# Optimization experiments

Hardware: AMD Instinct MI355X
Metric: run time of the kernel (lower is better)

Reference implementation:

```python
import math
import jax, jax.numpy as jnp
import numpy as np

D_MODEL = 512
NHEAD = 8
D_HEAD = D_MODEL // NHEAD
ATTN_TEMP = 1.0
B, LQ, LK = 2, 2048, 4096


def _linear_params(key, d_in, d_out):
    kw, kb = jax.random.split(key)
    bound = 1.0 / math.sqrt(d_in)
    W = jax.random.uniform(kw, (d_out, d_in), jnp.float32, -bound, bound)
    b = jax.random.uniform(kb, (d_out,), jnp.float32, -bound, bound)
    return W, b


def setup_inputs() -> dict:
    key = jax.random.key(0)
    ks = jax.random.split(key, 8)
    q = jax.random.normal(ks[0], (B, LQ, D_MODEL), jnp.float32)
    kv = jax.random.normal(ks[1], (B, LK, D_MODEL), jnp.float32)
    key_gate = jax.random.uniform(ks[2], (B, LK), jnp.float32)
    key_mask = jax.random.randint(ks[3], (B, LK), 0, 2, jnp.int32)
    Wq, bq = _linear_params(ks[4], D_MODEL, D_MODEL)
    Wk, bk = _linear_params(ks[5], D_MODEL, D_MODEL)
    Wv, bv = _linear_params(ks[6], D_MODEL, D_MODEL)
    Wo, bo = _linear_params(ks[7], D_MODEL, D_MODEL)
    return {"q": q, "kv": kv, "key_gate": key_gate, "key_mask": key_mask,
            "Wq": Wq, "bq": bq, "Wk": Wk, "bk": bk,
            "Wv": Wv, "bv": bv, "Wo": Wo, "bo": bo}


def reference(q, kv, key_gate, key_mask, Wq, bq, Wk, bk, Wv, bv, Wo, bo):
    Bq, Lq, _ = q.shape
    _, Lk, _ = kv.shape
    # projections -> (B, H, L, Dh)
    qp = (q @ Wq.T + bq).reshape(Bq, Lq, NHEAD, D_HEAD).transpose(0, 2, 1, 3)
    kp = (kv @ Wk.T + bk).reshape(Bq, Lk, NHEAD, D_HEAD).transpose(0, 2, 1, 3)
    vp = (kv @ Wv.T + bv).reshape(Bq, Lk, NHEAD, D_HEAD).transpose(0, 2, 1, 3)
    # scores: (B, H, Lq, Lk)
    scores = jnp.einsum('bhqd,bhkd->bhqk', qp, kp) / (math.sqrt(D_HEAD) * ATTN_TEMP)
    log_gate = jnp.log(jnp.clip(key_gate, 1e-6, None))  # (B, Lk)
    scores = scores + log_gate[:, None, None, :]
    pad = (key_mask == 0)[:, None, None, :]
    scores = jnp.where(pad, -jnp.inf, scores)
    attn = jax.nn.softmax(scores, axis=-1)  # dropout is identity in eval
    out = jnp.einsum('bhqk,bhkd->bhqd', attn, vp)
    out = out.transpose(0, 2, 1, 3).reshape(Bq, Lq, D_MODEL)
    return out @ Wo.T + bo
```

## Files before the change

### kernel.cpp

```cpp
#include <hip/hip_runtime.h>
#include <hip/hip_bf16.h>


using bf16   = __hip_bfloat16;
using bf16x8 = __attribute__((ext_vector_type(8))) short;
using f32x4  = __attribute__((ext_vector_type(4))) float;
using f32x16 = __attribute__((ext_vector_type(16))) float;
using uint4v = __attribute__((ext_vector_type(4))) unsigned int;

#define MFMA16(a, b, c) __builtin_amdgcn_mfma_f32_16x16x32_bf16((a), (b), (c), 0, 0, 0)
#define MFMA32(a, b, c) __builtin_amdgcn_mfma_f32_32x32x16_bf16((a), (b), (c), 0, 0, 0)

__device__ __forceinline__ bf16x8 load8(const bf16* p) {
    return *reinterpret_cast<const bf16x8*>(p);
}
__device__ __forceinline__ short f2bf(float x) {
    bf16 h = __float2bfloat16(x);
    return *reinterpret_cast<short*>(&h);
}

__global__ void cvt_x(const float* __restrict__ q, const float* __restrict__ kv,
                      bf16* __restrict__ qb, bf16* __restrict__ kvb) {
    int i = blockIdx.x * blockDim.x + threadIdx.x;
    const float* src; bf16* dst; int j;
    if (i < 524288) { src = q;  dst = qb;  j = i; }
    else            { src = kv; dst = kvb; j = i - 524288; }
    float4 v = reinterpret_cast<const float4*>(src)[j];
    ushort4 o;
    o.x = (unsigned short)f2bf(v.x);
    o.y = (unsigned short)f2bf(v.y);
    o.z = (unsigned short)f2bf(v.z);
    o.w = (unsigned short)f2bf(v.w);
    reinterpret_cast<ushort4*>(dst)[j] = o;
}

__global__ void cvt_w(const float* __restrict__ a, const float* __restrict__ b,
                      const float* __restrict__ c, const float* __restrict__ d,
                      bf16* __restrict__ oa, bf16* __restrict__ ob,
                      bf16* __restrict__ oc, bf16* __restrict__ od) {
    int i = blockIdx.x * blockDim.x + threadIdx.x;
    int t = i >> 16, j = i & 65535;
    const float* src = (t == 0) ? a : (t == 1) ? b : (t == 2) ? c : d;
    bf16*        dst = (t == 0) ? oa : (t == 1) ? ob : (t == 2) ? oc : od;
    float4 v = reinterpret_cast<const float4*>(src)[j];
    ushort4 o;
    o.x = (unsigned short)f2bf(v.x);
    o.y = (unsigned short)f2bf(v.y);
    o.z = (unsigned short)f2bf(v.z);
    o.w = (unsigned short)f2bf(v.w);
    reinterpret_cast<ushort4*>(dst)[j] = o;
}

__global__ void prep_gate_kernel(const float* __restrict__ gate,
                                 const int* __restrict__ mask,
                                 float* __restrict__ g, int n) {
    int i = blockIdx.x * blockDim.x + threadIdx.x;
    if (i < n) {
        float gv = fmaxf(gate[i], 1e-6f);
        g[i] = mask[i] ? log2f(gv) : -1e30f;
    }
}

__device__ __forceinline__ void proj_body(const bf16* __restrict__ X,
                                          const bf16* __restrict__ W,
                                          const float* __restrict__ bias,
                                          void* __restrict__ Cout,
                                          int mode, int L, int mb, bf16* Ws) {
    const int tid  = threadIdx.x;
    const int wave = tid >> 6;
    const int lane = tid & 63;
    const int li   = lane & 15;
    const int quad = lane >> 4;
    const int n0   = blockIdx.x * 64;
    const int m0   = mb * 128 + wave * 32;

    f32x4 zero = {0.f, 0.f, 0.f, 0.f};
    f32x4 acc[2][4];
    for (int mt = 0; mt < 2; ++mt)
        for (int t = 0; t < 4; ++t) acc[mt][t] = zero;

    const bf16* x0 = X + (size_t)(m0 + li) * 512;
    const bf16* x1 = X + (size_t)(m0 + 16 + li) * 512;

    for (int p = 0; p < 2; ++p) {
        __syncthreads();
        for (int i = 0; i < 8; ++i) {
            const int c  = i * 256 + tid;
            const int cr = c >> 5;
            const int kc = (c & 31) * 8;
            *reinterpret_cast<bf16x8*>(&Ws[cr * 264 + kc]) =
                load8(W + (size_t)(n0 + cr) * 512 + p * 256 + kc);
        }
        __syncthreads();

        for (int k0 = 0; k0 < 256; k0 += 32) {
            bf16x8 a0 = load8(x0 + p * 256 + k0 + quad * 8);
            bf16x8 a1 = load8(x1 + p * 256 + k0 + quad * 8);
            for (int t = 0; t < 4; ++t) {
                bf16x8 w8 = load8(&Ws[(t * 16 + li) * 264 + k0 + quad * 8]);
                acc[0][t] = MFMA16(a0, w8, acc[0][t]);
                acc[1][t] = MFMA16(a1, w8, acc[1][t]);
            }
        }
    }

    for (int t = 0; t < 4; ++t) {
        const int col = n0 + t * 16 + li;
        const float bcol = bias[col];
        for (int mt = 0; mt < 2; ++mt) {
            for (int r = 0; r < 4; ++r) {
                const int row = m0 + mt * 16 + quad * 4 + r;
                const float v = acc[mt][t][r] + bcol;
                if (mode == 0) {
                    ((float*)Cout)[(size_t)row * 512 + col] = v;
                } else {
                    const int bb2 = row / L;
                    const int i   = row - bb2 * L;
                    const int hh  = col >> 6;
                    const int dh  = col & 63;
                    const int bh  = bb2 * 8 + hh;
                    size_t idx;
                    if (mode == 1) {
                        idx = ((size_t)bh * L + i) * 64 + dh;
                    } else if (mode == 3) {
                        idx = ((((size_t)bh * 128 + (i >> 5)) * 4 + (dh >> 4)) * 64
                               + ((dh >> 3) & 1) * 32 + (i & 31)) * 8 + (dh & 7);
                    } else {
                        idx = (((((size_t)bh * 128 + (i >> 5)) * 2 + (dh >> 5)) * 2
                               + ((i >> 4) & 1)) * 64 + ((i >> 3) & 1) * 32 + (dh & 31)) * 8
                              + (i & 7);
                    }
                    ((bf16*)Cout)[idx] = __float2bfloat16(v);
                }
            }
        }
    }
}

__global__ void proj_qkv(const bf16* __restrict__ qb, const bf16* __restrict__ kvb,
                         const bf16* __restrict__ Wq, const float* __restrict__ bq,
                         const bf16* __restrict__ Wk, const float* __restrict__ bk,
                         const bf16* __restrict__ Wv, const float* __restrict__ bv,
                         bf16* __restrict__ qp, bf16* __restrict__ kf,
                         bf16* __restrict__ vf) {
    __shared__ alignas(16) bf16 Ws[64 * 264];
    const int my = blockIdx.y;
    if (my < 32)      proj_body(qb,  Wq, bq, qp, 1, 2048, my,      Ws);
    else if (my < 96) proj_body(kvb, Wk, bk, kf, 3, 4096, my - 32, Ws);
    else              proj_body(kvb, Wv, bv, vf, 4, 4096, my - 96, Ws);
}

__global__ void proj_o(const bf16* __restrict__ op, const bf16* __restrict__ Wo,
                       const float* __restrict__ bo, float* __restrict__ out) {
    __shared__ alignas(16) bf16 Ws[64 * 264];
    proj_body(op, Wo, bo, out, 0, 1, blockIdx.y, Ws);
}

__global__ __launch_bounds__(256, 2)
void attn_kernel(const bf16* __restrict__ qp, const bf16* __restrict__ kf,
                 const bf16* __restrict__ vf, const float* __restrict__ g2,
                 float* __restrict__ Opart, float* __restrict__ lpart) {
    const int tid  = threadIdx.x;
    const int wave = tid >> 6;
    const int lane = tid & 63;
    const int ql   = lane & 31;
    const int hi   = lane >> 5;

    const int bx = blockIdx.x;
    const int sp = bx & 3;
    const int qt = (bx >> 2) & 7;
    const int h  = (bx >> 5) & 7;
    const int b  = bx >> 8;
    const int bh = b * 8 + h;
    const int q0 = qt * 256 + wave * 64;

    bf16x8 bq[2][4];
    const bf16* qb = qp + ((size_t)bh * 2048 + q0 + ql) * 64 + hi * 8;
    #pragma unroll
    for (int sub = 0; sub < 2; ++sub)
        #pragma unroll
        for (int ds = 0; ds < 4; ++ds)
            bq[sub][ds] = load8(qb + sub * 2048 + ds * 16);

    f32x16 od[2][2];
    #pragma unroll
    for (int sub = 0; sub < 2; ++sub)
        #pragma unroll
        for (int t = 0; t < 2; ++t)
            #pragma unroll
            for (int r = 0; r < 16; ++r) od[sub][t][r] = 0.f;
    float lsum[2] = {0.f, 0.f};

    const bf16* kbase = kf + (size_t)bh * 262144 + (size_t)sp * 65536 + lane * 8;
    const bf16* vbase = vf + (size_t)bh * 262144 + (size_t)sp * 65536 + lane * 8;
    const float* gbase = g2 + (size_t)b * 4096 + sp * 1024 + hi * 4;

    const float SC = 0.18033688011112042f;

    bf16x8 ka0 = load8(kbase);
    bf16x8 ka1 = load8(kbase + 512);
    bf16x8 ka2 = load8(kbase + 1024);
    bf16x8 ka3 = load8(kbase + 1536);

    for (int kt = 0; kt < 32; ++kt) {
        const bf16* vp = vbase + (size_t)kt * 2048;
        bf16x8 bv00 = load8(vp);
        bf16x8 bv01 = load8(vp + 512);
        bf16x8 bv10 = load8(vp + 1024);
        bf16x8 bv11 = load8(vp + 1536);
        const float* gp = gbase + kt * 32;
        f32x4 gv0 = *(const f32x4*)(gp);
        f32x4 gv1 = *(const f32x4*)(gp + 8);
        f32x4 gv2 = *(const f32x4*)(gp + 16);
        f32x4 gv3 = *(const f32x4*)(gp + 24);
        float gl[16];
        #pragma unroll
        for (int c = 0; c < 4; ++c) {
            gl[c] = gv0[c]; gl[4 + c] = gv1[c]; gl[8 + c] = gv2[c]; gl[12 + c] = gv3[c];
        }

        bf16x8 pa[2][2];
        #pragma unroll
        for (int sub = 0; sub < 2; ++sub) {
            f32x16 sacc;
            #pragma unroll
            for (int r = 0; r < 16; ++r) sacc[r] = 0.f;
            sacc = MFMA32(ka0, bq[sub][0], sacc);
            sacc = MFMA32(ka1, bq[sub][1], sacc);
            sacc = MFMA32(ka2, bq[sub][2], sacc);
            sacc = MFMA32(ka3, bq[sub][3], sacc);

            float p[16];
            #pragma unroll
            for (int r = 0; r < 16; ++r)
                p[r] = __builtin_amdgcn_exp2f(fmaf(sacc[r], SC, gl[r]));

            unsigned w[8];
            #pragma unroll
            for (int i = 0; i < 8; ++i)
                asm("v_cvt_pk_bf16_f32 %0, %1, %2"
                    : "=v"(w[i]) : "v"(p[2 * i]), "v"(p[2 * i + 1]));

            #pragma unroll
            for (int st = 1; st < 16; st <<= 1)
                #pragma unroll
                for (int r = 0; r < 16; r += 2 * st) p[r] += p[r + st];
            lsum[sub] += p[0];

            asm("v_permlane32_swap_b32 %0, %1" : "+v"(w[0]), "+v"(w[2]));
            asm("v_permlane32_swap_b32 %0, %1" : "+v"(w[1]), "+v"(w[3]));
            asm("v_permlane32_swap_b32 %0, %1" : "+v"(w[4]), "+v"(w[6]));
            asm("v_permlane32_swap_b32 %0, %1" : "+v"(w[5]), "+v"(w[7]));
            uint4v u0 = {w[0], w[1], w[2], w[3]};
            uint4v u1 = {w[4], w[5], w[6], w[7]};
            pa[sub][0] = __builtin_bit_cast(bf16x8, u0);
            pa[sub][1] = __builtin_bit_cast(bf16x8, u1);
        }

        const int ktn = kt < 31 ? kt + 1 : 31;
        const bf16* kp_n = kbase + (size_t)ktn * 2048;
        bf16x8 kn0 = load8(kp_n);
        bf16x8 kn1 = load8(kp_n + 512);
        bf16x8 kn2 = load8(kp_n + 1024);
        bf16x8 kn3 = load8(kp_n + 1536);

        od[0][0] = MFMA32(pa[0][0], bv00, od[0][0]);
        od[0][0] = MFMA32(pa[0][1], bv01, od[0][0]);
        od[0][1] = MFMA32(pa[0][0], bv10, od[0][1]);
        od[0][1] = MFMA32(pa[0][1], bv11, od[0][1]);
        od[1][0] = MFMA32(pa[1][0], bv00, od[1][0]);
        od[1][0] = MFMA32(pa[1][1], bv01, od[1][0]);
        od[1][1] = MFMA32(pa[1][0], bv10, od[1][1]);
        od[1][1] = MFMA32(pa[1][1], bv11, od[1][1]);

        ka0 = kn0; ka1 = kn1; ka2 = kn2; ka3 = kn3;
    }

    float l0 = lsum[0] + __shfl_xor(lsum[0], 32);
    float l1 = lsum[1] + __shfl_xor(lsum[1], 32);

    float* ob = Opart + ((size_t)(bh * 2048 + q0) * 4 + sp) * 64;
    #pragma unroll
    for (int sub = 0; sub < 2; ++sub)
        #pragma unroll
        for (int t = 0; t < 2; ++t)
            #pragma unroll
            for (int r = 0; r < 16; ++r) {
                const int qq = sub * 32 + (r & 3) + 8 * (r >> 2) + hi * 4;
                ob[(size_t)qq * 256 + t * 32 + ql] = od[sub][t][r];
            }
    if (lane < 32) {
        lpart[((size_t)(bh * 2048 + q0 + lane)) * 4 + sp]      = l0;
        lpart[((size_t)(bh * 2048 + q0 + 32 + lane)) * 4 + sp] = l1;
    }
}

__global__ void attn_combine(const float* __restrict__ Opart,
                             const float* __restrict__ lpart,
                             bf16* __restrict__ op) {
    const int gidx = blockIdx.x * 256 + threadIdx.x;
    const int row  = gidx >> 2;
    const int c0   = (gidx & 3) * 16;

    float acc[16];
    #pragma unroll
    for (int j = 0; j < 16; ++j) acc[j] = 0.f;
    float L = 0.f;
    for (int s = 0; s < 4; ++s) {
        const float* src = Opart + ((size_t)row * 4 + s) * 64 + c0;
        const float4 v0 = reinterpret_cast<const float4*>(src)[0];
        const float4 v1 = reinterpret_cast<const float4*>(src)[1];
        const float4 v2 = reinterpret_cast<const float4*>(src)[2];
        const float4 v3 = reinterpret_cast<const float4*>(src)[3];
        acc[0] += v0.x; acc[1] += v0.y; acc[2]  += v0.z; acc[3]  += v0.w;
        acc[4] += v1.x; acc[5] += v1.y; acc[6]  += v1.z; acc[7]  += v1.w;
        acc[8] += v2.x; acc[9] += v2.y; acc[10] += v2.z; acc[11] += v2.w;
        acc[12] += v3.x; acc[13] += v3.y; acc[14] += v3.z; acc[15] += v3.w;
        L += lpart[(size_t)row * 4 + s];
    }
    const float invL = 1.0f / L;

    const int bh = row >> 11;
    const int q  = row & 2047;
    const int bb = bh >> 3;
    const int hh = bh & 7;
    bf16* dst = op + ((size_t)bb * 2048 + q) * 512 + hh * 64 + c0;
    bf16x8 r0, r1;
    #pragma unroll
    for (int j = 0; j < 8; ++j) {
        r0[j] = f2bf(acc[j] * invL);
        r1[j] = f2bf(acc[8 + j] * invL);
    }
    *reinterpret_cast<bf16x8*>(dst)     = r0;
    *reinterpret_cast<bf16x8*>(dst + 8) = r1;
}

extern "C" void kernel_launch(void* const* d_in, const int* in_sizes, int n_in,
                              void* d_out, int out_size, void* d_ws, size_t ws_size,
                              hipStream_t stream) {
    const float* q    = (const float*)d_in[0];
    const float* kv   = (const float*)d_in[1];
    const float* gate = (const float*)d_in[2];
    const int*   mask = (const int*)d_in[3];
    const float* Wq = (const float*)d_in[4];  const float* bq = (const float*)d_in[5];
    const float* Wk = (const float*)d_in[6];  const float* bk = (const float*)d_in[7];
    const float* Wv = (const float*)d_in[8];  const float* bv = (const float*)d_in[9];
    const float* Wo = (const float*)d_in[10]; const float* bo = (const float*)d_in[11];
    float* out = (float*)d_out;

    char* ws = (char*)d_ws;
    float* g2  = (float*)ws;
    bf16* Wqb  = (bf16*)(ws + (1u  << 20));
    bf16* Wkb  = (bf16*)(ws + (1u  << 20) + (512u << 10));
    bf16* Wvb  = (bf16*)(ws + (2u  << 20));
    bf16* Wob  = (bf16*)(ws + (2u  << 20) + (512u << 10));
    bf16* qb   = (bf16*)(ws + (3u  << 20));
    bf16* kvb  = (bf16*)(ws + (7u  << 20));
    bf16* qp   = (bf16*)(ws + (15u << 20));
    bf16* kf   = (bf16*)(ws + (19u << 20));
    bf16* vf   = (bf16*)(ws + (27u << 20));
    bf16* op   = (bf16*)(ws + (35u << 20));
    float* Opart = (float*)(ws + (39u << 20));
    float* lpart = (float*)(ws + (71u << 20));

    prep_gate_kernel<<<32, 256, 0, stream>>>(gate, mask, g2, 2 * 4096);
    cvt_x<<<6144, 256, 0, stream>>>(q, kv, qb, kvb);
    cvt_w<<<1024, 256, 0, stream>>>(Wq, Wk, Wv, Wo, Wqb, Wkb, Wvb, Wob);

    proj_qkv<<<dim3(8, 160), 256, 0, stream>>>(qb, kvb, Wqb, bq, Wkb, bk,
                                               Wvb, bv, qp, kf, vf);

    attn_kernel<<<512, 256, 0, stream>>>(qp, kf, vf, g2, Opart, lpart);
    attn_combine<<<512, 256, 0, stream>>>(Opart, lpart, op);

    proj_o<<<dim3(8, 32), 256, 0, stream>>>(op, Wob, bo, out);
}
```

Measured before the change: 189.7 us.

## Fuse conversion kernels, stage projection stores via LDS, remap blocks, reorder attention MFMAs

Merges the three preprocessing kernels (input cast, weight cast, gate log2/mask) into one launch with vectorized gate handling. Projection epilogues now stage bf16 results in shared memory and write them out with coalesced 16-byte stores instead of scattered 2-byte stores. Block indices for the projection and attention kernels are remapped so neighbouring blocks share operands, aiming at better cache locality. In the attention loop both QK MFMA chains are issued together under raised wave priority, and the next K prefetch is moved before the softmax. Together these reduce launch count and store inefficiency but add extra barriers and LDS traffic in the projection epilogue.

```diff
diff --git a/kernel.cpp b/kernel.cpp
--- a/kernel.cpp
+++ b/kernel.cpp
@@ -14,50 +14,44 @@
 __device__ __forceinline__ bf16x8 load8(const bf16* p) {
     return *reinterpret_cast<const bf16x8*>(p);
 }
-__device__ __forceinline__ short f2bf(float x) {
+__device__ __forceinline__ unsigned short f2bf(float x) {
     bf16 h = __float2bfloat16(x);
-    return *reinterpret_cast<short*>(&h);
-}
-
-__global__ void cvt_x(const float* __restrict__ q, const float* __restrict__ kv,
-                      bf16* __restrict__ qb, bf16* __restrict__ kvb) {
-    int i = blockIdx.x * blockDim.x + threadIdx.x;
-    const float* src; bf16* dst; int j;
-    if (i < 524288) { src = q;  dst = qb;  j = i; }
-    else            { src = kv; dst = kvb; j = i - 524288; }
-    float4 v = reinterpret_cast<const float4*>(src)[j];
-    ushort4 o;
-    o.x = (unsigned short)f2bf(v.x);
-    o.y = (unsigned short)f2bf(v.y);
-    o.z = (unsigned short)f2bf(v.z);
-    o.w = (unsigned short)f2bf(v.w);
-    reinterpret_cast<ushort4*>(dst)[j] = o;
-}
-
-__global__ void cvt_w(const float* __restrict__ a, const float* __restrict__ b,
-                      const float* __restrict__ c, const float* __restrict__ d,
-                      bf16* __restrict__ oa, bf16* __restrict__ ob,
-                      bf16* __restrict__ oc, bf16* __restrict__ od) {
-    int i = blockIdx.x * blockDim.x + threadIdx.x;
-    int t = i >> 16, j = i & 65535;
-    const float* src = (t == 0) ? a : (t == 1) ? b : (t == 2) ? c : d;
-    bf16*        dst = (t == 0) ? oa : (t == 1) ? ob : (t == 2) ? oc : od;
-    float4 v = reinterpret_cast<const float4*>(src)[j];
-    ushort4 o;
-    o.x = (unsigned short)f2bf(v.x);
-    o.y = (unsigned short)f2bf(v.y);
-    o.z = (unsigned short)f2bf(v.z);
-    o.w = (unsigned short)f2bf(v.w);
-    reinterpret_cast<ushort4*>(dst)[j] = o;
-}
-
-__global__ void prep_gate_kernel(const float* __restrict__ gate,
-                                 const int* __restrict__ mask,
-                                 float* __restrict__ g, int n) {
-    int i = blockIdx.x * blockDim.x + threadIdx.x;
-    if (i < n) {
-        float gv = fmaxf(gate[i], 1e-6f);
-        g[i] = mask[i] ? log2f(gv) : -1e30f;
+    return *reinterpret_cast<unsigned short*>(&h);
+}
+
+__global__ void cvt_all(const float* __restrict__ q, const float* __restrict__ kv,
+                        const float* __restrict__ Wq, const float* __restrict__ Wk,
+                        const float* __restrict__ Wv, const float* __restrict__ Wo,
+                        const float* __restrict__ gate, const int* __restrict__ mask,
+                        bf16* __restrict__ qb, bf16* __restrict__ kvb,
+                        bf16* __restrict__ Wqb, bf16* __restrict__ Wkb,
+                        bf16* __restrict__ Wvb, bf16* __restrict__ Wob,
+                        float* __restrict__ g2) {
+    const int i = blockIdx.x * 256 + threadIdx.x;
+    if (i < 1835008) {
+        const float* src; bf16* dst; int j;
+        if (i < 524288)       { src = q;  dst = qb;  j = i; }
+        else if (i < 1572864) { src = kv; dst = kvb; j = i - 524288; }
+        else {
+            const int i2 = i - 1572864;
+            const int t = i2 >> 16; j = i2 & 65535;
+            src = (t == 0) ? Wq : (t == 1) ? Wk : (t == 2) ? Wv : Wo;
+            dst = (t == 0) ? Wqb : (t == 1) ? Wkb : (t == 2) ? Wvb : Wob;
+        }
+        float4 v = reinterpret_cast<const float4*>(src)[j];
+        ushort4 o;
+        o.x = f2bf(v.x); o.y = f2bf(v.y); o.z = f2bf(v.z); o.w = f2bf(v.w);
+        reinterpret_cast<ushort4*>(dst)[j] = o;
+    } else {
+        const int u = i - 1835008;
+        float4 gv = reinterpret_cast<const float4*>(gate)[u];
+        int4   mv = reinterpret_cast<const int4*>(mask)[u];
+        float4 o;
+        o.x = mv.x ? log2f(fmaxf(gv.x, 1e-6f)) : -1e30f;
+        o.y = mv.y ? log2f(fmaxf(gv.y, 1e-6f)) : -1e30f;
+        o.z = mv.z ? log2f(fmaxf(gv.z, 1e-6f)) : -1e30f;
+        o.w = mv.w ? log2f(fmaxf(gv.w, 1e-6f)) : -1e30f;
+        reinterpret_cast<float4*>(g2)[u] = o;
     }
 }
 
@@ -65,13 +59,14 @@
                                           const bf16* __restrict__ W,
                                           const float* __restrict__ bias,
                                           void* __restrict__ Cout,
-                                          int mode, int L, int mb, bf16* Ws) {
+                                          int mode, int L, int mb, int nb,
+                                          bf16* Ws) {
     const int tid  = threadIdx.x;
     const int wave = tid >> 6;
     const int lane = tid & 63;
     const int li   = lane & 15;
     const int quad = lane >> 4;
-    const int n0   = blockIdx.x * 64;
+    const int n0   = nb * 64;
     const int m0   = mb * 128 + wave * 32;
 
     f32x4 zero = {0.f, 0.f, 0.f, 0.f};
@@ -104,36 +99,50 @@
         }
     }
 
-    for (int t = 0; t < 4; ++t) {
-        const int col = n0 + t * 16 + li;
-        const float bcol = bias[col];
-        for (int mt = 0; mt < 2; ++mt) {
-            for (int r = 0; r < 4; ++r) {
-                const int row = m0 + mt * 16 + quad * 4 + r;
-                const float v = acc[mt][t][r] + bcol;
-                if (mode == 0) {
-                    ((float*)Cout)[(size_t)row * 512 + col] = v;
-                } else {
-                    const int bb2 = row / L;
-                    const int i   = row - bb2 * L;
-                    const int hh  = col >> 6;
-                    const int dh  = col & 63;
-                    const int bh  = bb2 * 8 + hh;
-                    size_t idx;
-                    if (mode == 1) {
-                        idx = ((size_t)bh * L + i) * 64 + dh;
-                    } else if (mode == 3) {
-                        idx = ((((size_t)bh * 128 + (i >> 5)) * 4 + (dh >> 4)) * 64
-                               + ((dh >> 3) & 1) * 32 + (i & 31)) * 8 + (dh & 7);
-                    } else {
-                        idx = (((((size_t)bh * 128 + (i >> 5)) * 2 + (dh >> 5)) * 2
-                               + ((i >> 4) & 1)) * 64 + ((i >> 3) & 1) * 32 + (dh & 31)) * 8
-                              + (i & 7);
-                    }
-                    ((bf16*)Cout)[idx] = __float2bfloat16(v);
+    if (mode == 0) {
+        for (int t = 0; t < 4; ++t) {
+            const int col = n0 + t * 16 + li;
+            const float bcol = bias[col];
+            for (int mt = 0; mt < 2; ++mt)
+                for (int r = 0; r < 4; ++r) {
+                    const int row = m0 + mt * 16 + quad * 4 + r;
+                    ((float*)Cout)[(size_t)row * 512 + col] = acc[mt][t][r] + bcol;
                 }
-            }
-        }
+        }
+    } else {
+        __syncthreads();
+        bf16* slab = Ws + wave * 2048;
+        #pragma unroll
+        for (int t = 0; t < 4; ++t) {
+            const float bcol = bias[n0 + t * 16 + li];
+            #pragma unroll
+            for (int mt = 0; mt < 2; ++mt)
+                #pragma unroll
+                for (int r = 0; r < 4; ++r) {
+                    const float v = acc[mt][t][r] + bcol;
+                    int lidx;
+                    if (mode == 1)
+                        lidx = (mt * 16 + quad * 4 + r) * 64 + t * 16 + li;
+                    else if (mode == 3)
+                        lidx = t * 512 + (li >> 3) * 256 + (mt * 16 + quad * 4 + r) * 8 + (li & 7);
+                    else
+                        lidx = (t >> 1) * 1024 + mt * 512 + (quad >> 1) * 256
+                             + ((t & 1) * 16 + li) * 8 + (quad & 1) * 4 + r;
+                    slab[lidx] = __float2bfloat16(v);
+                }
+        }
+        __syncthreads();
+        const int bb2 = m0 / L;
+        const int i0  = m0 - bb2 * L;
+        const int hh  = n0 >> 6;
+        const int bh  = bb2 * 8 + hh;
+        bf16* base;
+        if (mode == 1) base = (bf16*)Cout + ((size_t)bh * L + i0) * 64;
+        else           base = (bf16*)Cout + (size_t)bh * L * 64 + (size_t)(i0 >> 5) * 2048;
+        #pragma unroll
+        for (int s = 0; s < 4; ++s)
+            *reinterpret_cast<bf16x8*>(base + s * 512 + lane * 8) =
+                load8(&slab[s * 512 + lane * 8]);
     }
 }
 
@@ -144,16 +153,21 @@
                          bf16* __restrict__ qp, bf16* __restrict__ kf,
                          bf16* __restrict__ vf) {
     __shared__ alignas(16) bf16 Ws[64 * 264];
-    const int my = blockIdx.y;
-    if (my < 32)      proj_body(qb,  Wq, bq, qp, 1, 2048, my,      Ws);
-    else if (my < 96) proj_body(kvb, Wk, bk, kf, 3, 4096, my - 32, Ws);
-    else              proj_body(kvb, Wv, bv, vf, 4, 4096, my - 96, Ws);
+    const int l   = blockIdx.x;
+    const int w   = l & 63;
+    const int myy = (l >> 6) * 8 + (w & 7);
+    const int nb  = w >> 3;
+    if (myy < 32)      proj_body(qb,  Wq, bq, qp, 1, 2048, myy,      nb, Ws);
+    else if (myy < 96) proj_body(kvb, Wk, bk, kf, 3, 4096, myy - 32, nb, Ws);
+    else               proj_body(kvb, Wv, bv, vf, 4, 4096, myy - 96, nb, Ws);
 }
 
 __global__ void proj_o(const bf16* __restrict__ op, const bf16* __restrict__ Wo,
                        const float* __restrict__ bo, float* __restrict__ out) {
     __shared__ alignas(16) bf16 Ws[64 * 264];
-    proj_body(op, Wo, bo, out, 0, 1, blockIdx.y, Ws);
+    const int l = blockIdx.x;
+    const int w = l & 63;
+    proj_body(op, Wo, bo, out, 0, 1, (l >> 6) * 8 + (w & 7), w >> 3, Ws);
 }
 
 __global__ __launch_bounds__(256, 2)
@@ -166,21 +180,21 @@
     const int ql   = lane & 31;
     const int hi   = lane >> 5;
 
-    const int bx = blockIdx.x;
-    const int sp = bx & 3;
-    const int qt = (bx >> 2) & 7;
-    const int h  = (bx >> 5) & 7;
-    const int b  = bx >> 8;
-    const int bh = b * 8 + h;
+    const int id = blockIdx.x;
+    const int qt = (id >> 3) & 7;
+    const int gg = ((id >> 6) << 3) | (id & 7);
+    const int bh = gg >> 2;
+    const int sp = gg & 3;
+    const int b  = bh >> 3;
     const int q0 = qt * 256 + wave * 64;
 
     bf16x8 bq[2][4];
-    const bf16* qb = qp + ((size_t)bh * 2048 + q0 + ql) * 64 + hi * 8;
+    const bf16* qbp = qp + ((size_t)bh * 2048 + q0 + ql) * 64 + hi * 8;
     #pragma unroll
     for (int sub = 0; sub < 2; ++sub)
         #pragma unroll
         for (int ds = 0; ds < 4; ++ds)
-            bq[sub][ds] = load8(qb + sub * 2048 + ds * 16);
+            bq[sub][ds] = load8(qbp + sub * 2048 + ds * 16);
 
     f32x16 od[2][2];
     #pragma unroll
@@ -213,65 +227,69 @@
         f32x4 gv1 = *(const f32x4*)(gp + 8);
         f32x4 gv2 = *(const f32x4*)(gp + 16);
         f32x4 gv3 = *(const f32x4*)(gp + 24);
-        float gl[16];
-        #pragma unroll
-        for (int c = 0; c < 4; ++c) {
-            gl[c] = gv0[c]; gl[4 + c] = gv1[c]; gl[8 + c] = gv2[c]; gl[12 + c] = gv3[c];
-        }
-
-        bf16x8 pa[2][2];
-        #pragma unroll
-        for (int sub = 0; sub < 2; ++sub) {
-            f32x16 sacc;
-            #pragma unroll
-            for (int r = 0; r < 16; ++r) sacc[r] = 0.f;
-            sacc = MFMA32(ka0, bq[sub][0], sacc);
-            sacc = MFMA32(ka1, bq[sub][1], sacc);
-            sacc = MFMA32(ka2, bq[sub][2], sacc);
-            sacc = MFMA32(ka3, bq[sub][3], sacc);
-
+
+        f32x16 s0, s1;
+        #pragma unroll
+        for (int r = 0; r < 16; ++r) { s0[r] = 0.f; s1[r] = 0.f; }
+        __builtin_amdgcn_s_setprio(1);
+        s0 = MFMA32(ka0, bq[0][0], s0);
+        s0 = MFMA32(ka1, bq[0][1], s0);
+        s0 = MFMA32(ka2, bq[0][2], s0);
+        s0 = MFMA32(ka3, bq[0][3], s0);
+        s1 = MFMA32(ka0, bq[1][0], s1);
+        s1 = MFMA32(ka1, bq[1][1], s1);
+        s1 = MFMA32(ka2, bq[1][2], s1);
+        s1 = MFMA32(ka3, bq[1][3], s1);
+        __builtin_amdgcn_s_setprio(0);
+
+        const int ktn = kt < 31 ? kt + 1 : 31;
+        const bf16* kp_n = kbase + (size_t)ktn * 2048;
+        bf16x8 kn0 = load8(kp_n);
+        bf16x8 kn1 = load8(kp_n + 512);
+        bf16x8 kn2 = load8(kp_n + 1024);
+        bf16x8 kn3 = load8(kp_n + 1536);
+
+        bf16x8 pa00, pa01, pa10, pa11;
+        auto softmax = [&](const f32x16& sacc, float& lacc, bf16x8& plo, bf16x8& phi) {
             float p[16];
             #pragma unroll
-            for (int r = 0; r < 16; ++r)
-                p[r] = __builtin_amdgcn_exp2f(fmaf(sacc[r], SC, gl[r]));
-
+            for (int r = 0; r < 16; ++r) {
+                const float gl = (r < 4) ? gv0[r & 3] : (r < 8) ? gv1[r & 3]
+                               : (r < 12) ? gv2[r & 3] : gv3[r & 3];
+                p[r] = __builtin_amdgcn_exp2f(fmaf(sacc[r], SC, gl));
+            }
             unsigned w[8];
             #pragma unroll
             for (int i = 0; i < 8; ++i)
                 asm("v_cvt_pk_bf16_f32 %0, %1, %2"
                     : "=v"(w[i]) : "v"(p[2 * i]), "v"(p[2 * i + 1]));
-
             #pragma unroll
             for (int st = 1; st < 16; st <<= 1)
                 #pragma unroll
                 for (int r = 0; r < 16; r += 2 * st) p[r] += p[r + st];
-            lsum[sub] += p[0];
-
+            lacc += p[0];
             asm("v_permlane32_swap_b32 %0, %1" : "+v"(w[0]), "+v"(w[2]));
             asm("v_permlane32_swap_b32 %0, %1" : "+v"(w[1]), "+v"(w[3]));
             asm("v_permlane32_swap_b32 %0, %1" : "+v"(w[4]), "+v"(w[6]));
             asm("v_permlane32_swap_b32 %0, %1" : "+v"(w[5]), "+v"(w[7]));
             uint4v u0 = {w[0], w[1], w[2], w[3]};
             uint4v u1 = {w[4], w[5], w[6], w[7]};
-            pa[sub][0] = __builtin_bit_cast(bf16x8, u0);
-            pa[sub][1] = __builtin_bit_cast(bf16x8, u1);
-        }
-
-        const int ktn = kt < 31 ? kt + 1 : 31;
-        const bf16* kp_n = kbase + (size_t)ktn * 2048;
-        bf16x8 kn0 = load8(kp_n);
-        bf16x8 kn1 = load8(kp_n + 512);
-        bf16x8 kn2 = load8(kp_n + 1024);
-        bf16x8 kn3 = load8(kp_n + 1536);
-
-        od[0][0] = MFMA32(pa[0][0], bv00, od[0][0]);
-        od[0][0] = MFMA32(pa[0][1], bv01, od[0][0]);
-        od[0][1] = MFMA32(pa[0][0], bv10, od[0][1]);
-        od[0][1] = MFMA32(pa[0][1], bv11, od[0][1]);
-        od[1][0] = MFMA32(pa[1][0], bv00, od[1][0]);
-        od[1][0] = MFMA32(pa[1][1], bv01, od[1][0]);
-        od[1][1] = MFMA32(pa[1][0], bv10, od[1][1]);
-        od[1][1] = MFMA32(pa[1][1], bv11, od[1][1]);
+            plo = __builtin_bit_cast(bf16x8, u0);
+            phi = __builtin_bit_cast(bf16x8, u1);
+        };
+        softmax(s0, lsum[0], pa00, pa01);
+        softmax(s1, lsum[1], pa10, pa11);
+
+        __builtin_amdgcn_s_setprio(1);
+        od[0][0] = MFMA32(pa00, bv00, od[0][0]);
+        od[0][0] = MFMA32(pa01, bv01, od[0][0]);
+        od[0][1] = MFMA32(pa00, bv10, od[0][1]);
+        od[0][1] = MFMA32(pa01, bv11, od[0][1]);
+        od[1][0] = MFMA32(pa10, bv00, od[1][0]);
+        od[1][0] = MFMA32(pa11, bv01, od[1][0]);
+        od[1][1] = MFMA32(pa10, bv10, od[1][1]);
+        od[1][1] = MFMA32(pa11, bv11, od[1][1]);
+        __builtin_amdgcn_s_setprio(0);
 
         ka0 = kn0; ka1 = kn1; ka2 = kn2; ka3 = kn3;
     }
@@ -363,15 +381,14 @@
     float* Opart = (float*)(ws + (39u << 20));
     float* lpart = (float*)(ws + (71u << 20));
 
-    prep_gate_kernel<<<32, 256, 0, stream>>>(gate, mask, g2, 2 * 4096);
-    cvt_x<<<6144, 256, 0, stream>>>(q, kv, qb, kvb);
-    cvt_w<<<1024, 256, 0, stream>>>(Wq, Wk, Wv, Wo, Wqb, Wkb, Wvb, Wob);
-
-    proj_qkv<<<dim3(8, 160), 256, 0, stream>>>(qb, kvb, Wqb, bq, Wkb, bk,
-                                               Wvb, bv, qp, kf, vf);
+    cvt_all<<<7176, 256, 0, stream>>>(q, kv, Wq, Wk, Wv, Wo, gate, mask,
+                                      qb, kvb, Wqb, Wkb, Wvb, Wob, g2);
+
+    proj_qkv<<<1280, 256, 0, stream>>>(qb, kvb, Wqb, bq, Wkb, bk,
+                                       Wvb, bv, qp, kf, vf);
 
     attn_kernel<<<512, 256, 0, stream>>>(qp, kf, vf, g2, Opart, lpart);
     attn_combine<<<512, 256, 0, stream>>>(Opart, lpart, op);
 
-    proj_o<<<dim3(8, 32), 256, 0, stream>>>(op, Wob, bo, out);
-}
+    proj_o<<<256, 256, 0, stream>>>(op, Wob, bo, out);
+}
```

Result: faster. 179.0 us (-5.6%).
